# Optimization experiments

Hardware: AMD Instinct MI355X
Metric: run time of the kernel (lower is better)

## Reference

```python
import jax, jax.numpy as jnp
import numpy as np

TIME_PENALTY = 0.01
PONDER_EPS = 0.01
TIME_LIMIT = 16
BATCH, INPUT_SIZE, HIDDEN_SIZE = 4096, 1024, 1024


def setup_inputs() -> dict:
    key = jax.random.key(0)
    ks = jax.random.split(key, 8)
    s_in = 1.0 / np.sqrt(INPUT_SIZE + 1)
    s_h = 1.0 / np.sqrt(HIDDEN_SIZE)
    return {
        "inputs": jax.random.normal(ks[0], (BATCH, INPUT_SIZE), jnp.float32),
        "hidden": jax.random.normal(ks[1], (BATCH, HIDDEN_SIZE), jnp.float32),
        # RNNCell params (input size = INPUT_SIZE + 1 for the first-step flag)
        "W_ih": jax.random.uniform(ks[2], (HIDDEN_SIZE, INPUT_SIZE + 1), jnp.float32, -s_in, s_in),
        "b_ih": jax.random.uniform(ks[3], (HIDDEN_SIZE,), jnp.float32, -s_in, s_in),
        "W_hh": jax.random.uniform(ks[4], (HIDDEN_SIZE, HIDDEN_SIZE), jnp.float32, -s_h, s_h),
        "b_hh": jax.random.uniform(ks[5], (HIDDEN_SIZE,), jnp.float32, -s_h, s_h),
        # halting unit: Linear(hidden_size, 1), bias initialized to -1.0
        "W_halt": jax.random.uniform(ks[6], (1, HIDDEN_SIZE), jnp.float32, -s_h, s_h),
        "b_halt": jnp.full((1,), -1.0, jnp.float32),
    }


def _act_forward(inputs, hidden, W_ih, b_ih, W_hh, b_hh, W_halt, b_halt):
    B = inputs.shape[0]
    H = W_hh.shape[0]
    dt = inputs.dtype
    budget = jnp.asarray(1.0 - PONDER_EPS, dt)
    # input projection: the last input column is the first-step flag, so
    # step_inputs @ W_ih^T == inputs @ W_ih[:, :-1]^T + flag * W_ih[:, -1]
    x_base = inputs @ W_ih[:, :-1].T + b_ih  # (B, H)
    flag_col = W_ih[:, -1]                    # (H,)
    flags = (jnp.arange(TIME_LIMIT - 1) == 0).astype(dt)

    def step(carry, flag):
        h, halt_accum, cont, tot_h, tot_rem, tot_steps = carry
        h = jnp.tanh(x_base + flag * flag_col + h @ W_hh.T + b_hh)  # (B, H)
        step_halt = jax.nn.sigmoid(h @ W_halt.T + b_halt)           # (B, 1)
        masked_halt = jnp.where(cont, step_halt, 0.0)
        # halt accumulator is detached in the original (torch.no_grad)
        halt_accum = halt_accum + jax.lax.stop_gradient(masked_halt)
        ending = cont & (halt_accum + step_halt > budget)
        cont = cont & (~ending)
        tot_steps = tot_steps + cont.astype(dt)
        masked_rem = jnp.where(ending, 1.0 - halt_accum, 0.0)
        combined = masked_halt + masked_rem
        tot_h = tot_h + combined * h
        tot_rem = tot_rem + masked_halt
        return (h, halt_accum, cont, tot_h, tot_rem, tot_steps), None

    init = (
        hidden,
        jnp.zeros((B, 1), dt),
        jnp.ones((B, 1), bool),
        jnp.zeros((B, H), dt),
        jnp.zeros((B, 1), dt),
        jnp.zeros((B, 1), dt),
    )
    (h, halt_accum, cont, tot_h, tot_rem, tot_steps), _ = jax.lax.scan(step, init, flags)
    # for-else branch: elements still continuing after the loop get the remainder
    # (zero-contribution if everything halted early, matching the early break)
    tot_h = tot_h + jnp.where(cont, 1.0 - halt_accum, 0.0) * h
    ponder_cost = -TIME_PENALTY * tot_rem.mean()
    return tot_h, ponder_cost, tot_steps + 1.0


def reference(inputs, hidden, W_ih, b_ih, W_hh, b_hh, W_halt, b_halt):
    return _act_forward(inputs, hidden, W_ih, b_ih, W_hh, b_hh, W_halt, b_halt)
```

## Files before the change

kernel.cpp:

```cpp
#include <hip/hip_runtime.h>
#include <math.h>

#define BATCH 4096
#define HID   1024
#define KDIM  1024
#define NSTEP 15
#define KV    3072
#define NCHUNK (KV / 64)

#define TMM 128
#define TNN 64
#define LDAH 72

typedef _Float16 half8 __attribute__((ext_vector_type(8)));
typedef float floatx4 __attribute__((ext_vector_type(4)));

__device__ __forceinline__ _Float16 f16hi(float x) { return (_Float16)x; }

__device__ __forceinline__ void barrier_ls() {
    asm volatile("s_waitcnt lgkmcnt(0)" ::: "memory");
    __builtin_amdgcn_s_barrier();
    asm volatile("" ::: "memory");
}

__global__ __launch_bounds__(256) void setup_kernel(
    const float* __restrict__ W_ih, const float* __restrict__ W_hh,
    const float* __restrict__ inputs, const float* __restrict__ hidden,
    _Float16* __restrict__ B3ih, _Float16* __restrict__ B3hh,
    _Float16* __restrict__ Ihi, _Float16* __restrict__ Ilo,
    _Float16* __restrict__ Hhi, _Float16* __restrict__ Hlo,
    float* __restrict__ flagcol, int* __restrict__ list0, int* __restrict__ counts,
    float* __restrict__ halt_accum, float* __restrict__ tot_rem) {
    size_t idx = (size_t)blockIdx.x * 256 + threadIdx.x;
    {
        float x = inputs[idx];
        _Float16 h = f16hi(x);
        Ihi[idx] = h; Ilo[idx] = (_Float16)(x - (float)h);
        float y = hidden[idx];
        _Float16 g = f16hi(y);
        Hhi[idx] = g; Hlo[idx] = (_Float16)(y - (float)g);
    }
    if (idx < (size_t)KDIM * KDIM) {
        int n = (int)(idx >> 10), k = (int)(idx & 1023);
        float w = W_hh[idx];
        _Float16 hi = f16hi(w);
        _Float16 lo = (_Float16)(w - (float)hi);
        size_t base = (size_t)n * KV;
        B3hh[base + k] = hi; B3hh[base + 1024 + k] = lo; B3hh[base + 2048 + k] = hi;
        float w2 = W_ih[(size_t)n * 1025 + k];
        _Float16 hi2 = f16hi(w2);
        _Float16 lo2 = (_Float16)(w2 - (float)hi2);
        B3ih[base + k] = hi2; B3ih[base + 1024 + k] = lo2; B3ih[base + 2048 + k] = hi2;
    }
    if (idx < BATCH) { list0[idx] = idx; halt_accum[idx] = 0.f; tot_rem[idx] = 0.f; }
    if (idx < KDIM) flagcol[idx] = W_ih[idx * 1025 + 1024];
    if (idx < 16) counts[idx] = (idx == 0) ? BATCH : 0;
}

__global__ __launch_bounds__(256) void mfma_step_kernel(
    const _Float16* __restrict__ Ahi, const _Float16* __restrict__ Alo,
    const _Float16* __restrict__ B3, const float* __restrict__ bias,
    const float* __restrict__ xbase, const float* __restrict__ flagcol, float flag,
    const int* __restrict__ list, const int* __restrict__ pcount,
    float* __restrict__ hout, _Float16* __restrict__ houthi, _Float16* __restrict__ houtlo,
    float* __restrict__ xout, int mode) {
    int count = pcount ? *pcount : BATCH;
    int row0 = blockIdx.x * TMM;
    if (row0 >= count) return;
    int col0 = blockIdx.y * TNN;

    __shared__ _Float16 Asm[2][TMM][LDAH];
    __shared__ _Float16 Bsm[2][TNN][LDAH];

    int t = threadIdx.x;
    int lane = t & 63, w = t >> 6;
    int wm = (w & 1) * 64, wn = (w >> 1) * 32;

    int arw[4], aq8[4]; size_t aoff[4];
#pragma unroll
    for (int l = 0; l < 4; l++) {
        int q = t + l * 256;
        int r = q >> 3, qk = q & 7;
        arw[l] = r; aq8[l] = qk * 8;
        int rr = row0 + r;
        int g = (rr < count) ? (list ? list[rr] : rr) : 0;
        aoff[l] = (size_t)g * KDIM + qk * 8;
    }
    int brw[2], bq8[2]; size_t boff[2];
#pragma unroll
    for (int l = 0; l < 2; l++) {
        int q = t + l * 256;
        int r = q >> 3, qk = q & 7;
        brw[l] = r; bq8[l] = qk * 8;
        boff[l] = (size_t)(col0 + r) * KV + qk * 8;
    }

    floatx4 acc[4][2];
#pragma unroll
    for (int i = 0; i < 4; i++)
#pragma unroll
        for (int j = 0; j < 2; j++) acc[i][j] = (floatx4)(0.f);

    int l15 = lane & 15, l4 = lane >> 4;

    half8 avE[4], bvE[2];
    half8 avO[4], bvO[2];

#define ISSUE(avS, bvS, c) do {                                               \
        int k0v_ = (c) << 6;                                                  \
        const _Float16* Asrc_ = (k0v_ < 2048) ? Ahi : Alo;  \
        int kp_ = k0v_ & 1023;                                                \
        _Pragma("unroll")                                                     \
        for (int l = 0; l < 4; l++) avS[l] = *(const half8*)(Asrc_ + aoff[l] + kp_); \
        _Pragma("unroll")                                                     \
        for (int l = 0; l < 2; l++) bvS[l] = *(const half8*)(B3 + boff[l] + k0v_);   \
    } while (0)

#define LDSW(buf, avS, bvS) do {                                              \
        _Pragma("unroll")                                                     \
        for (int l = 0; l < 4; l++) *(half8*)(&Asm[buf][arw[l]][aq8[l]]) = avS[l]; \
        _Pragma("unroll")                                                     \
        for (int l = 0; l < 2; l++) *(half8*)(&Bsm[buf][brw[l]][bq8[l]]) = bvS[l]; \
    } while (0)

#define MFMA_CHUNK(buf) do {                                                  \
        _Pragma("unroll")                                                     \
        for (int ks = 0; ks < 2; ks++) {                                      \
            int ko = ks * 32 + l4 * 8;                                        \
            half8 af[4], bf[2];                                               \
            _Pragma("unroll")                                                 \
            for (int fi = 0; fi < 4; fi++)                                    \
                af[fi] = *(const half8*)(&Asm[buf][wm + fi * 16 + l15][ko]);  \
            _Pragma("unroll")                                                 \
            for (int fj = 0; fj < 2; fj++)                                    \
                bf[fj] = *(const half8*)(&Bsm[buf][wn + fj * 16 + l15][ko]);  \
            _Pragma("unroll")                                                 \
            for (int fi = 0; fi < 4; fi++)                                    \
                _Pragma("unroll")                                             \
                for (int fj = 0; fj < 2; fj++)                                \
                    acc[fi][fj] = __builtin_amdgcn_mfma_f32_16x16x32_f16(     \
                        af[fi], bf[fj], acc[fi][fj], 0, 0, 0);                \
        }                                                                     \
    } while (0)

    ISSUE(avE, bvE, 0);
    ISSUE(avO, bvO, 1);
    LDSW(0, avE, bvE);
    barrier_ls();

    for (int it = 0; it < NCHUNK; it += 2) {
        if (it + 2 < NCHUNK) ISSUE(avE, bvE, it + 2);
        MFMA_CHUNK(0);
        LDSW(1, avO, bvO);
        barrier_ls();
        if (it + 3 < NCHUNK) ISSUE(avO, bvO, it + 3);
        MFMA_CHUNK(1);
        if (it + 2 < NCHUNK) LDSW(0, avE, bvE);
        barrier_ls();
    }

#undef ISSUE
#undef LDSW
#undef MFMA_CHUNK

#pragma unroll
    for (int fi = 0; fi < 4; fi++) {
#pragma unroll
        for (int rr = 0; rr < 4; rr++) {
            int lm = wm + fi * 16 + l4 * 4 + rr;
            int grd = row0 + lm;
            if (grd >= count) continue;
            int g = list ? list[grd] : grd;
#pragma unroll
            for (int fj = 0; fj < 2; fj++) {
                int c = col0 + wn + fj * 16 + l15;
                float v = acc[fi][fj][rr];
                if (mode == 0) {
                    xout[(size_t)g * KDIM + c] = v + bias[c];
                } else {
                    v += xbase[(size_t)g * KDIM + c] + flag * flagcol[c] + bias[c];
                    v = tanhf(v);
                    hout[(size_t)g * KDIM + c] = v;
                    _Float16 hi = f16hi(v);
                    houthi[(size_t)g * KDIM + c] = hi;
                    houtlo[(size_t)g * KDIM + c] = (_Float16)(v - (float)hi);
                }
            }
        }
    }
}

__global__ __launch_bounds__(256) void halt_kernel(
    const float* __restrict__ h, const float* __restrict__ W_halt,
    const float* __restrict__ b_halt,
    const int* __restrict__ list, const int* __restrict__ pcount,
    int* __restrict__ list_next, int* __restrict__ pcount_next,
    float* __restrict__ halt_accum, float* __restrict__ tot_rem,
    float* __restrict__ tot_h, float* __restrict__ steps_out,
    int stepnum, int first) {
    int count = *pcount;
    int wid = threadIdx.x >> 6, lane = threadIdx.x & 63;
    int r = blockIdx.x * 4 + wid;
    if (r >= count) return;
    int row = list[r];
    const float* hr = h + (size_t)row * HID;

    float dot = 0.f;
#pragma unroll
    for (int q = 0; q < 4; q++) {
        int c = q * 256 + lane * 4;
        float4 hv = *(const float4*)(hr + c);
        float4 wv = *(const float4*)(W_halt + c);
        dot += hv.x * wv.x + hv.y * wv.y + hv.z * wv.z + hv.w * wv.w;
    }
#pragma unroll
    for (int off = 32; off > 0; off >>= 1) dot += __shfl_down(dot, off);

    float combined = 0.f;
    if (lane == 0) {
        float p = 1.f / (1.f + expf(-(dot + b_halt[0])));
        float S = halt_accum[row] + p;
        halt_accum[row] = S;
        tot_rem[row] += p;
        bool ending = (S + p) > 0.99f;
        if (ending) {
            combined = p + (1.f - S);
            steps_out[row] = (float)stepnum;
        } else {
            combined = p;
            int idx = atomicAdd(pcount_next, 1);
            list_next[idx] = row;
        }
    }
    combined = __shfl(combined, 0);

    float* th = tot_h + (size_t)row * HID;
#pragma unroll
    for (int q = 0; q < 4; q++) {
        int c = q * 256 + lane * 4;
        float4 hv = *(const float4*)(hr + c);
        float4 ov;
        if (first) {
            ov.x = combined * hv.x; ov.y = combined * hv.y;
            ov.z = combined * hv.z; ov.w = combined * hv.w;
        } else {
            ov = *(const float4*)(th + c);
            ov.x += combined * hv.x; ov.y += combined * hv.y;
            ov.z += combined * hv.z; ov.w += combined * hv.w;
        }
        *(float4*)(th + c) = ov;
    }
}

__global__ __launch_bounds__(256) void epilogue_kernel(
    const float* __restrict__ h, const int* __restrict__ list,
    const int* __restrict__ pcount, const float* __restrict__ halt_accum,
    const float* __restrict__ tot_rem,
    float* __restrict__ tot_h, float* __restrict__ steps_out,
    float* __restrict__ ponder) {
    if (blockIdx.x == 1024) {
        __shared__ float red[4];
        int t = threadIdx.x;
        float v = 0.f;
#pragma unroll
        for (int i = 0; i < 16; i++) v += tot_rem[t + i * 256];
#pragma unroll
        for (int off = 32; off > 0; off >>= 1) v += __shfl_down(v, off);
        int lane = t & 63, wid = t >> 6;
        if (lane == 0) red[wid] = v;
        __syncthreads();
        if (t == 0) ponder[0] = (red[0] + red[1] + red[2] + red[3]) * (-0.01f / 4096.f);
        return;
    }
    int count = *pcount;
    int wid = threadIdx.x >> 6, lane = threadIdx.x & 63;
    int r = blockIdx.x * 4 + wid;
    if (r >= count) return;
    int row = list[r];
    float cmb = 1.f - halt_accum[row];
    if (lane == 0) steps_out[row] = 16.f;
    const float* hr = h + (size_t)row * HID;
    float* th = tot_h + (size_t)row * HID;
#pragma unroll
    for (int q = 0; q < 4; q++) {
        int c = q * 256 + lane * 4;
        float4 hv = *(const float4*)(hr + c);
        float4 ov = *(const float4*)(th + c);
        ov.x += cmb * hv.x; ov.y += cmb * hv.y;
        ov.z += cmb * hv.z; ov.w += cmb * hv.w;
        *(float4*)(th + c) = ov;
    }
}

extern "C" void kernel_launch(void* const* d_in, const int* in_sizes, int n_in,
                              void* d_out, int out_size, void* d_ws, size_t ws_size,
                              hipStream_t stream) {
    const float* inputs = (const float*)d_in[0];
    const float* hidden = (const float*)d_in[1];
    const float* W_ih   = (const float*)d_in[2];
    const float* b_ih   = (const float*)d_in[3];
    const float* W_hh   = (const float*)d_in[4];
    const float* b_hh   = (const float*)d_in[5];
    const float* W_halt = (const float*)d_in[6];
    const float* b_halt = (const float*)d_in[7];
    float* out = (float*)d_out;

    float* ws = (float*)d_ws;
    const size_t NM = (size_t)BATCH * HID;
    float* xbase = ws;
    float* h     = xbase + NM;
    _Float16* B3ih = (_Float16*)(h + NM);
    _Float16* B3hh = B3ih + (size_t)HID * KV;
    _Float16* Ahi0 = B3hh + (size_t)HID * KV;
    _Float16* Alo0 = Ahi0 + NM;
    _Float16* Ahi1 = Alo0 + NM;
    _Float16* Alo1 = Ahi1 + NM;
    float* flagcol = (float*)(Alo1 + NM);
    float* halt_accum = flagcol + KDIM;
    float* tot_rem = halt_accum + BATCH;
    int* list0 = (int*)(tot_rem + BATCH);
    int* list1 = list0 + BATCH;
    int* counts = list1 + BATCH;

    _Float16* Ahi[2] = {Ahi0, Ahi1};
    _Float16* Alo[2] = {Alo0, Alo1};
    int* lists[2] = {list0, list1};

    float* tot_h = out;
    float* ponder = out + NM;
    float* steps_out = ponder + 1;

    setup_kernel<<<16384, 256, 0, stream>>>(W_ih, W_hh, inputs, hidden,
                                            B3ih, B3hh, Ahi1, Alo1, Ahi0, Alo0,
                                            flagcol, list0, counts, halt_accum, tot_rem);

    mfma_step_kernel<<<dim3(32, 16), 256, 0, stream>>>(
        Ahi1, Alo1, B3ih, b_ih, nullptr, nullptr, 0.f, nullptr, nullptr,
        nullptr, nullptr, nullptr, xbase, 0);

    for (int t = 0; t < NSTEP; t++) {
        mfma_step_kernel<<<dim3(32, 16), 256, 0, stream>>>(
            Ahi[t & 1], Alo[t & 1], B3hh, b_hh, xbase, flagcol,
            (t == 0) ? 1.f : 0.f, lists[t & 1], counts + t,
            h, Ahi[(t + 1) & 1], Alo[(t + 1) & 1], nullptr, 1);
        halt_kernel<<<1024, 256, 0, stream>>>(h, W_halt, b_halt,
                                              lists[t & 1], counts + t,
                                              lists[(t + 1) & 1], counts + t + 1,
                                              halt_accum, tot_rem, tot_h, steps_out,
                                              t + 1, (t == 0) ? 1 : 0);
    }
    epilogue_kernel<<<1025, 256, 0, stream>>>(h, lists[1], counts + 15,
                                              halt_accum, tot_rem, tot_h, steps_out, ponder);
}
```

Before: 738.5 us.

## Replace LDS-tiled GEMM with single-wave register-direct MFMA tiles

Rewrites the step GEMM so each 64-thread block computes a 64x64 tile, loading A and B fragments straight from global memory into registers. There is no shared-memory staging and no barriers, and a triple-buffered register prefetch hides load latency. This removes LDS traffic and barrier overhead, but loses the operand sharing across waves that the 128x64 block tile had, so global/L2 traffic goes up. Register pressure also rises, with 1024 single-wave blocks at launch_bounds(64,1).

```diff
diff --git a/kernel.cpp b/kernel.cpp
--- a/kernel.cpp
+++ b/kernel.cpp
@@ -8,20 +8,11 @@
 #define KV    3072
 #define NCHUNK (KV / 64)
 
-#define TMM 128
-#define TNN 64
-#define LDAH 72
 
 typedef _Float16 half8 __attribute__((ext_vector_type(8)));
 typedef float floatx4 __attribute__((ext_vector_type(4)));
 
 __device__ __forceinline__ _Float16 f16hi(float x) { return (_Float16)x; }
-
-__device__ __forceinline__ void barrier_ls() {
-    asm volatile("s_waitcnt lgkmcnt(0)" ::: "memory");
-    __builtin_amdgcn_s_barrier();
-    asm volatile("" ::: "memory");
-}
 
 __global__ __launch_bounds__(256) void setup_kernel(
     const float* __restrict__ W_ih, const float* __restrict__ W_hh,
@@ -57,7 +48,7 @@
     if (idx < 16) counts[idx] = (idx == 0) ? BATCH : 0;
 }
 
-__global__ __launch_bounds__(256) void mfma_step_kernel(
+__global__ __launch_bounds__(64, 1) void mfma_step_kernel(
     const _Float16* __restrict__ Ahi, const _Float16* __restrict__ Alo,
     const _Float16* __restrict__ B3, const float* __restrict__ bias,
     const float* __restrict__ xbase, const float* __restrict__ flagcol, float flag,
@@ -65,115 +56,86 @@
     float* __restrict__ hout, _Float16* __restrict__ houthi, _Float16* __restrict__ houtlo,
     float* __restrict__ xout, int mode) {
     int count = pcount ? *pcount : BATCH;
-    int row0 = blockIdx.x * TMM;
+    int bx = blockIdx.x >> 4, by = blockIdx.x & 15;
+    int row0 = bx * 64;
     if (row0 >= count) return;
-    int col0 = blockIdx.y * TNN;
-
-    __shared__ _Float16 Asm[2][TMM][LDAH];
-    __shared__ _Float16 Bsm[2][TNN][LDAH];
-
-    int t = threadIdx.x;
-    int lane = t & 63, w = t >> 6;
-    int wm = (w & 1) * 64, wn = (w >> 1) * 32;
-
-    int arw[4], aq8[4]; size_t aoff[4];
-#pragma unroll
-    for (int l = 0; l < 4; l++) {
-        int q = t + l * 256;
-        int r = q >> 3, qk = q & 7;
-        arw[l] = r; aq8[l] = qk * 8;
-        int rr = row0 + r;
-        int g = (rr < count) ? (list ? list[rr] : rr) : 0;
-        aoff[l] = (size_t)g * KDIM + qk * 8;
-    }
-    int brw[2], bq8[2]; size_t boff[2];
-#pragma unroll
-    for (int l = 0; l < 2; l++) {
-        int q = t + l * 256;
-        int r = q >> 3, qk = q & 7;
-        brw[l] = r; bq8[l] = qk * 8;
-        boff[l] = (size_t)(col0 + r) * KV + qk * 8;
-    }
-
-    floatx4 acc[4][2];
+    int col0 = by * 64;
+
+    int lane = threadIdx.x;
+    int l15 = lane & 15, l4 = lane >> 4;
+    int koff = l4 * 8;
+
+    size_t abase[4], bbase[4];
+#pragma unroll
+    for (int f = 0; f < 4; f++) {
+        int grow = row0 + f * 16 + l15;
+        int g = (grow < count) ? (list ? list[grow] : grow) : 0;
+        abase[f] = (size_t)g * KDIM + koff;
+        bbase[f] = (size_t)(col0 + f * 16 + l15) * KV + koff;
+    }
+
+    floatx4 acc[4][4];
 #pragma unroll
     for (int i = 0; i < 4; i++)
 #pragma unroll
-        for (int j = 0; j < 2; j++) acc[i][j] = (floatx4)(0.f);
-
-    int l15 = lane & 15, l4 = lane >> 4;
-
-    half8 avE[4], bvE[2];
-    half8 avO[4], bvO[2];
-
-#define ISSUE(avS, bvS, c) do {                                               \
+        for (int j = 0; j < 4; j++) acc[i][j] = (floatx4)(0.f);
+
+    half8 avA[4][2], bvA[4][2];
+    half8 avB[4][2], bvB[4][2];
+    half8 avC[4][2], bvC[4][2];
+
+#define ISSUE(av, bv, c) do {                                                 \
         int k0v_ = (c) << 6;                                                  \
-        const _Float16* Asrc_ = (k0v_ < 2048) ? Ahi : Alo;  \
+        const _Float16* As_ = (k0v_ < 2048) ? Ahi : Alo;  \
         int kp_ = k0v_ & 1023;                                                \
         _Pragma("unroll")                                                     \
-        for (int l = 0; l < 4; l++) avS[l] = *(const half8*)(Asrc_ + aoff[l] + kp_); \
+        for (int f = 0; f < 4; f++) {                                         \
+            _Pragma("unroll")                                                 \
+            for (int ks = 0; ks < 2; ks++) {                                  \
+                av[f][ks] = *(const half8*)(As_ + abase[f] + kp_ + ks * 32);  \
+                bv[f][ks] = *(const half8*)(B3 + bbase[f] + k0v_ + ks * 32);  \
+            }                                                                 \
+        }                                                                     \
+    } while (0)
+
+#define MFMA_SET(av, bv) do {                                                 \
         _Pragma("unroll")                                                     \
-        for (int l = 0; l < 2; l++) bvS[l] = *(const half8*)(B3 + boff[l] + k0v_);   \
-    } while (0)
-
-#define LDSW(buf, avS, bvS) do {                                              \
-        _Pragma("unroll")                                                     \
-        for (int l = 0; l < 4; l++) *(half8*)(&Asm[buf][arw[l]][aq8[l]]) = avS[l]; \
-        _Pragma("unroll")                                                     \
-        for (int l = 0; l < 2; l++) *(half8*)(&Bsm[buf][brw[l]][bq8[l]]) = bvS[l]; \
-    } while (0)
-
-#define MFMA_CHUNK(buf) do {                                                  \
-        _Pragma("unroll")                                                     \
-        for (int ks = 0; ks < 2; ks++) {                                      \
-            int ko = ks * 32 + l4 * 8;                                        \
-            half8 af[4], bf[2];                                               \
-            _Pragma("unroll")                                                 \
-            for (int fi = 0; fi < 4; fi++)                                    \
-                af[fi] = *(const half8*)(&Asm[buf][wm + fi * 16 + l15][ko]);  \
-            _Pragma("unroll")                                                 \
-            for (int fj = 0; fj < 2; fj++)                                    \
-                bf[fj] = *(const half8*)(&Bsm[buf][wn + fj * 16 + l15][ko]);  \
+        for (int ks = 0; ks < 2; ks++)                                        \
             _Pragma("unroll")                                                 \
             for (int fi = 0; fi < 4; fi++)                                    \
                 _Pragma("unroll")                                             \
-                for (int fj = 0; fj < 2; fj++)                                \
+                for (int fj = 0; fj < 4; fj++)                                \
                     acc[fi][fj] = __builtin_amdgcn_mfma_f32_16x16x32_f16(     \
-                        af[fi], bf[fj], acc[fi][fj], 0, 0, 0);                \
-        }                                                                     \
+                        av[fi][ks], bv[fj][ks], acc[fi][fj], 0, 0, 0);        \
     } while (0)
 
-    ISSUE(avE, bvE, 0);
-    ISSUE(avO, bvO, 1);
-    LDSW(0, avE, bvE);
-    barrier_ls();
-
-    for (int it = 0; it < NCHUNK; it += 2) {
-        if (it + 2 < NCHUNK) ISSUE(avE, bvE, it + 2);
-        MFMA_CHUNK(0);
-        LDSW(1, avO, bvO);
-        barrier_ls();
-        if (it + 3 < NCHUNK) ISSUE(avO, bvO, it + 3);
-        MFMA_CHUNK(1);
-        if (it + 2 < NCHUNK) LDSW(0, avE, bvE);
-        barrier_ls();
+    ISSUE(avA, bvA, 0);
+    ISSUE(avB, bvB, 1);
+    ISSUE(avC, bvC, 2);
+
+    for (int it = 0; it < NCHUNK; it += 3) {
+        MFMA_SET(avA, bvA);
+        if (it + 3 < NCHUNK) ISSUE(avA, bvA, it + 3);
+        MFMA_SET(avB, bvB);
+        if (it + 4 < NCHUNK) ISSUE(avB, bvB, it + 4);
+        MFMA_SET(avC, bvC);
+        if (it + 5 < NCHUNK) ISSUE(avC, bvC, it + 5);
     }
 
 #undef ISSUE
-#undef LDSW
-#undef MFMA_CHUNK
+#undef MFMA_SET
 
 #pragma unroll
     for (int fi = 0; fi < 4; fi++) {
 #pragma unroll
         for (int rr = 0; rr < 4; rr++) {
-            int lm = wm + fi * 16 + l4 * 4 + rr;
+            int lm = fi * 16 + l4 * 4 + rr;
             int grd = row0 + lm;
             if (grd >= count) continue;
             int g = list ? list[grd] : grd;
 #pragma unroll
-            for (int fj = 0; fj < 2; fj++) {
-                int c = col0 + wn + fj * 16 + l15;
+            for (int fj = 0; fj < 4; fj++) {
+                int c = col0 + fj * 16 + l15;
                 float v = acc[fi][fj][rr];
                 if (mode == 0) {
                     xout[(size_t)g * KDIM + c] = v + bias[c];
@@ -334,12 +296,12 @@
                                             B3ih, B3hh, Ahi1, Alo1, Ahi0, Alo0,
                                             flagcol, list0, counts, halt_accum, tot_rem);
 
-    mfma_step_kernel<<<dim3(32, 16), 256, 0, stream>>>(
+    mfma_step_kernel<<<1024, 64, 0, stream>>>(
         Ahi1, Alo1, B3ih, b_ih, nullptr, nullptr, 0.f, nullptr, nullptr,
         nullptr, nullptr, nullptr, xbase, 0);
 
     for (int t = 0; t < NSTEP; t++) {
-        mfma_step_kernel<<<dim3(32, 16), 256, 0, stream>>>(
+        mfma_step_kernel<<<1024, 64, 0, stream>>>(
             Ahi[t & 1], Alo[t & 1], B3hh, b_hh, xbase, flagcol,
             (t == 0) ? 1.f : 0.f, lists[t & 1], counts + t,
             h, Ahi[(t + 1) & 1], Alo[(t + 1) & 1], nullptr, 1);
```

After: 954.5 us. +29.3%, slower.

## Stage GEMM tiles via direct global-to-LDS loads with XOR-swizzled layout

Applied to the files above, without the earlier changes.

Replaces the register-staged global load and LDS store pipeline with direct global_load_lds transfers into unpadded shared-memory tiles. An XOR swizzle on the 16-byte column slot replaces the row padding as the way to avoid LDS bank conflicts on the MFMA fragment reads. The loop becomes a simple double buffer with one __syncthreads per chunk. This saves VGPRs and the LDS write instructions, but relies on __syncthreads draining the async LDS loads and drops the two-chunk-ahead register prefetch.

```diff
diff --git a/kernel.cpp b/kernel.cpp
--- a/kernel.cpp
+++ b/kernel.cpp
@@ -1,5 +1,6 @@
 #include <hip/hip_runtime.h>
 #include <math.h>
+#include <stdint.h>
 
 #define BATCH 4096
 #define HID   1024
@@ -8,19 +9,17 @@
 #define KV    3072
 #define NCHUNK (KV / 64)
 
-#define TMM 128
-#define TNN 64
-#define LDAH 72
 
 typedef _Float16 half8 __attribute__((ext_vector_type(8)));
 typedef float floatx4 __attribute__((ext_vector_type(4)));
 
+typedef __attribute__((address_space(3))) uint32_t lds_u32_t;
+typedef __attribute__((address_space(1))) const uint32_t gl_u32_t;
+
 __device__ __forceinline__ _Float16 f16hi(float x) { return (_Float16)x; }
 
-__device__ __forceinline__ void barrier_ls() {
-    asm volatile("s_waitcnt lgkmcnt(0)" ::: "memory");
-    __builtin_amdgcn_s_barrier();
-    asm volatile("" ::: "memory");
+__device__ __forceinline__ void gl_lds16(const _Float16* g, _Float16* l) {
+    __builtin_amdgcn_global_load_lds((gl_u32_t*)g, (lds_u32_t*)l, 16, 0, 0);
 }
 
 __global__ __launch_bounds__(256) void setup_kernel(
@@ -65,34 +64,32 @@
     float* __restrict__ hout, _Float16* __restrict__ houthi, _Float16* __restrict__ houtlo,
     float* __restrict__ xout, int mode) {
     int count = pcount ? *pcount : BATCH;
-    int row0 = blockIdx.x * TMM;
+    int row0 = blockIdx.x * 128;
     if (row0 >= count) return;
-    int col0 = blockIdx.y * TNN;
-
-    __shared__ _Float16 Asm[2][TMM][LDAH];
-    __shared__ _Float16 Bsm[2][TNN][LDAH];
+    int col0 = blockIdx.y * 64;
+
+    __shared__ _Float16 AsmL[2 * 128 * 64];
+    __shared__ _Float16 BsmL[2 * 64 * 64];
 
     int t = threadIdx.x;
     int lane = t & 63, w = t >> 6;
     int wm = (w & 1) * 64, wn = (w >> 1) * 32;
-
-    int arw[4], aq8[4]; size_t aoff[4];
-#pragma unroll
-    for (int l = 0; l < 4; l++) {
-        int q = t + l * 256;
-        int r = q >> 3, qk = q & 7;
-        arw[l] = r; aq8[l] = qk * 8;
-        int rr = row0 + r;
-        int g = (rr < count) ? (list ? list[rr] : rr) : 0;
-        aoff[l] = (size_t)g * KDIM + qk * 8;
-    }
-    int brw[2], bq8[2]; size_t boff[2];
-#pragma unroll
-    for (int l = 0; l < 2; l++) {
-        int q = t + l * 256;
-        int r = q >> 3, qk = q & 7;
-        brw[l] = r; bq8[l] = qk * 8;
-        boff[l] = (size_t)(col0 + r) * KV + qk * 8;
+    int l15 = lane & 15, l4 = lane >> 4;
+
+    int swg = ((lane & 7) ^ (lane >> 3)) << 3;
+    size_t aoff[4];
+#pragma unroll
+    for (int j = 0; j < 4; j++) {
+        int r = w * 32 + j * 8 + (lane >> 3);
+        int grow = row0 + r;
+        int g = (grow < count) ? (list ? list[grow] : grow) : 0;
+        aoff[j] = (size_t)g * KDIM + swg;
+    }
+    size_t boff[2];
+#pragma unroll
+    for (int j = 0; j < 2; j++) {
+        int r = w * 16 + j * 8 + (lane >> 3);
+        boff[j] = (size_t)(col0 + r) * KV + swg;
     }
 
     floatx4 acc[4][2];
@@ -101,39 +98,33 @@
 #pragma unroll
         for (int j = 0; j < 2; j++) acc[i][j] = (floatx4)(0.f);
 
-    int l15 = lane & 15, l4 = lane >> 4;
-
-    half8 avE[4], bvE[2];
-    half8 avO[4], bvO[2];
-
-#define ISSUE(avS, bvS, c) do {                                               \
+#define STAGE(buf, c) do {                                                    \
         int k0v_ = (c) << 6;                                                  \
-        const _Float16* Asrc_ = (k0v_ < 2048) ? Ahi : Alo;  \
+        const _Float16* As_ = (k0v_ < 2048) ? Ahi : Alo;  \
         int kp_ = k0v_ & 1023;                                                \
         _Pragma("unroll")                                                     \
-        for (int l = 0; l < 4; l++) avS[l] = *(const half8*)(Asrc_ + aoff[l] + kp_); \
+        for (int j = 0; j < 4; j++)                                           \
+            gl_lds16(As_ + aoff[j] + kp_,                                     \
+                     &AsmL[(buf) * 8192 + (w * 4 + j) * 512]);                \
         _Pragma("unroll")                                                     \
-        for (int l = 0; l < 2; l++) bvS[l] = *(const half8*)(B3 + boff[l] + k0v_);   \
-    } while (0)
-
-#define LDSW(buf, avS, bvS) do {                                              \
-        _Pragma("unroll")                                                     \
-        for (int l = 0; l < 4; l++) *(half8*)(&Asm[buf][arw[l]][aq8[l]]) = avS[l]; \
-        _Pragma("unroll")                                                     \
-        for (int l = 0; l < 2; l++) *(half8*)(&Bsm[buf][brw[l]][bq8[l]]) = bvS[l]; \
+        for (int j = 0; j < 2; j++)                                           \
+            gl_lds16(B3 + boff[j] + k0v_,                                     \
+                     &BsmL[(buf) * 4096 + (w * 2 + j) * 512]);                \
     } while (0)
 
 #define MFMA_CHUNK(buf) do {                                                  \
         _Pragma("unroll")                                                     \
         for (int ks = 0; ks < 2; ks++) {                                      \
-            int ko = ks * 32 + l4 * 8;                                        \
+            int slot = (((ks * 4 + l4) ^ (l15 & 7)) << 3);                    \
             half8 af[4], bf[2];                                               \
             _Pragma("unroll")                                                 \
             for (int fi = 0; fi < 4; fi++)                                    \
-                af[fi] = *(const half8*)(&Asm[buf][wm + fi * 16 + l15][ko]);  \
+                af[fi] = *(const half8*)(&AsmL[(buf) * 8192 +                 \
+                              (wm + fi * 16 + l15) * 64 + slot]);             \
             _Pragma("unroll")                                                 \
             for (int fj = 0; fj < 2; fj++)                                    \
-                bf[fj] = *(const half8*)(&Bsm[buf][wn + fj * 16 + l15][ko]);  \
+                bf[fj] = *(const half8*)(&BsmL[(buf) * 4096 +                 \
+                              (wn + fj * 16 + l15) * 64 + slot]);             \
             _Pragma("unroll")                                                 \
             for (int fi = 0; fi < 4; fi++)                                    \
                 _Pragma("unroll")                                             \
@@ -143,24 +134,18 @@
         }                                                                     \
     } while (0)
 
-    ISSUE(avE, bvE, 0);
-    ISSUE(avO, bvO, 1);
-    LDSW(0, avE, bvE);
-    barrier_ls();
-
-    for (int it = 0; it < NCHUNK; it += 2) {
-        if (it + 2 < NCHUNK) ISSUE(avE, bvE, it + 2);
-        MFMA_CHUNK(0);
-        LDSW(1, avO, bvO);
-        barrier_ls();
-        if (it + 3 < NCHUNK) ISSUE(avO, bvO, it + 3);
-        MFMA_CHUNK(1);
-        if (it + 2 < NCHUNK) LDSW(0, avE, bvE);
-        barrier_ls();
-    }
-
-#undef ISSUE
-#undef LDSW
+    STAGE(0, 0);
+    __syncthreads();
+
+    int p = 0;
+    for (int it = 0; it < NCHUNK; it++) {
+        if (it + 1 < NCHUNK) STAGE(p ^ 1, it + 1);
+        MFMA_CHUNK(p);
+        __syncthreads();
+        p ^= 1;
+    }
+
+#undef STAGE
 #undef MFMA_CHUNK
 
 #pragma unroll
```

New measurement: 879.0 us. 1.19x slower.
